# Kernel optimization log

Hardware: AMD Instinct MI355X
Metric: run time of the kernel (lower is better)

The kernel has to match this reference:

```python
import jax, jax.numpy as jnp
import numpy as np

N_NODES = 100000
N_EDGES = 3200000
DIM_IN = 256
DIM_OUT = 256


def setup_inputs() -> dict:
    key = jax.random.key(0)
    k1, k2, k3, k4, k5 = jax.random.split(key, 5)
    x = jax.random.normal(k1, (N_NODES, DIM_IN), dtype=jnp.float32)
    adj_rows = jax.random.randint(k2, (N_EDGES,), 0, N_NODES, dtype=jnp.int64)
    adj_cols = jax.random.randint(k3, (N_EDGES,), 0, N_NODES, dtype=jnp.int64)
    adj_vals = jax.random.uniform(k4, (N_EDGES,), dtype=jnp.float32)
    # torch Linear weight: [dim_out, dim_in]
    W = jax.random.normal(k5, (DIM_OUT, DIM_IN), dtype=jnp.float32) * (1.0 / np.sqrt(DIM_IN))
    return {"x": x, "adj_rows": adj_rows, "adj_cols": adj_cols, "adj_vals": adj_vals, "W": W}


def reference(x, adj_rows, adj_cols, adj_vals, W):
    # h = Linear(x) with no bias -> x @ W.T  : [N, dim_out]
    h = jnp.einsum('nd,od->no', x, W)
    # sparse.mm(adjacency, h): out[r] = sum_{edges e with row r} val[e] * h[col[e]]
    msgs = adj_vals[:, None] * h[adj_cols]            # [E, dim_out]
    out = jax.ops.segment_sum(msgs, adj_rows, num_segments=N_NODES)
    return out
```

## Files before the change

### kernel.cpp

```cpp
#include <hip/hip_runtime.h>
#include <hip/hip_bf16.h>

#define DIM 256
#define GRP 8
#define CAP8 88
#define OVF_CAP 65536

typedef short s16x8 __attribute__((ext_vector_type(8)));
typedef float f32x4 __attribute__((ext_vector_type(4)));

__device__ inline unsigned short f32_bf16_rne(float f) {
    unsigned u = __float_as_uint(f);
    u += 0x7FFFu + ((u >> 16) & 1u);
    return (unsigned short)(u >> 16);
}
__device__ inline float bf16_f32(unsigned short h) {
    return __uint_as_float(((unsigned)h) << 16);
}
__device__ inline float4 bf16x4_f32(uint2 p) {
    float4 r;
    r.x = __uint_as_float(p.x << 16);
    r.y = __uint_as_float(p.x & 0xFFFF0000u);
    r.z = __uint_as_float(p.y << 16);
    r.w = __uint_as_float(p.y & 0xFFFF0000u);
    return r;
}

__global__ __launch_bounds__(256) void prep_w(const float* __restrict__ W,
                                              unsigned short* __restrict__ Wh) {
    int i = blockIdx.x * 256 + threadIdx.x;
    Wh[i] = f32_bf16_rne(W[i]);
}

__global__ __launch_bounds__(256) void gemm_mfma(const float* __restrict__ X,
                                                 const unsigned short* __restrict__ Wh,
                                                 unsigned short* __restrict__ H, int N) {
    __shared__ __align__(16) unsigned short xh[64 * 32];
    __shared__ __align__(16) unsigned short xl[64 * 32];

    const int tid = threadIdx.x;
    const int lane = tid & 63;
    const int wv = tid >> 6;
    const int bm = blockIdx.x * 64;

    const int srow = tid & 63;
    const int schunk = tid >> 6;
    const int grow = bm + srow;
    const bool rowok = grow < N;
    const float* xsrc = X + (size_t)grow * DIM + schunk * 8;
    const int swch = srow * 4 + (schunk ^ ((srow >> 1) & 3));

    const int frow = lane & 15;
    const int fch = lane >> 4;

    f32x4 acc[4][4] = {};

    for (int k0 = 0; k0 < DIM; k0 += 32) {
        float v[8];
        if (rowok) {
            float4 a = *(const float4*)(xsrc + k0);
            float4 b = *(const float4*)(xsrc + k0 + 4);
            v[0] = a.x; v[1] = a.y; v[2] = a.z; v[3] = a.w;
            v[4] = b.x; v[5] = b.y; v[6] = b.z; v[7] = b.w;
        } else {
#pragma unroll
            for (int e = 0; e < 8; ++e) v[e] = 0.f;
        }
        unsigned hh[8], ll[8];
#pragma unroll
        for (int e = 0; e < 8; ++e) {
            unsigned short hu = f32_bf16_rne(v[e]);
            hh[e] = hu;
            ll[e] = f32_bf16_rne(v[e] - bf16_f32(hu));
        }
        uint4 hv = make_uint4(hh[0] | (hh[1] << 16), hh[2] | (hh[3] << 16),
                              hh[4] | (hh[5] << 16), hh[6] | (hh[7] << 16));
        uint4 lv = make_uint4(ll[0] | (ll[1] << 16), ll[2] | (ll[3] << 16),
                              ll[4] | (ll[5] << 16), ll[6] | (ll[7] << 16));
        ((uint4*)xh)[swch] = hv;
        ((uint4*)xl)[swch] = lv;
        __syncthreads();

        s16x8 ah[4], al[4], bh[4];
#pragma unroll
        for (int i = 0; i < 4; ++i) {
            int row = i * 16 + frow;
            int rch = row * 4 + (fch ^ ((row >> 1) & 3));
            ah[i] = __builtin_bit_cast(s16x8, ((const uint4*)xh)[rch]);
            al[i] = __builtin_bit_cast(s16x8, ((const uint4*)xl)[rch]);
        }
#pragma unroll
        for (int j = 0; j < 4; ++j) {
            size_t off = (size_t)(wv * 64 + j * 16 + frow) * DIM + k0 + fch * 8;
            bh[j] = __builtin_bit_cast(s16x8, *(const uint4*)(Wh + off));
        }
#pragma unroll
        for (int i = 0; i < 4; ++i)
#pragma unroll
            for (int j = 0; j < 4; ++j) {
                acc[i][j] = __builtin_amdgcn_mfma_f32_16x16x32_bf16(ah[i], bh[j], acc[i][j], 0, 0, 0);
                acc[i][j] = __builtin_amdgcn_mfma_f32_16x16x32_bf16(al[i], bh[j], acc[i][j], 0, 0, 0);
            }
        __syncthreads();
    }

#pragma unroll
    for (int i = 0; i < 4; ++i)
#pragma unroll
        for (int r = 0; r < 4; ++r) {
            int row = bm + i * 16 + fch * 4 + r;
            if (row < N) {
#pragma unroll
                for (int j = 0; j < 4; ++j)
                    H[(size_t)row * DIM + wv * 64 + j * 16 + frow] = f32_bf16_rne(acc[i][j][r]);
            }
        }
}

__global__ __launch_bounds__(256) void scatter_bucket8(const int* __restrict__ rows,
                                                       const int* __restrict__ cols,
                                                       const float* __restrict__ vals,
                                                       int* __restrict__ cur,
                                                       unsigned long long* __restrict__ buckets,
                                                       uint4* __restrict__ ovf,
                                                       int* __restrict__ ovf_cnt,
                                                       int nE, int B8) {
    unsigned xcd;
    asm volatile("s_getreg_b32 %0, hwreg(HW_REG_XCC_ID)" : "=s"(xcd));
    xcd &= 7;

    int i = blockIdx.x * 256 + threadIdx.x;
    int st = gridDim.x * 256;
    for (int e = i; e < nE; e += st) {
        int r = rows[e];
        unsigned c = (unsigned)cols[e];
        unsigned vb = __float_as_uint(vals[e]);
        int cell = (int)xcd * B8 + (r >> 3);
        int p = atomicAdd(&cur[cell], 1);
        if (p < CAP8) {
            unsigned lo = c | ((unsigned)(r & 7) << 17);
            buckets[(size_t)cell * CAP8 + p] = (unsigned long long)lo | ((unsigned long long)vb << 32);
        } else {
            int q = atomicAdd(ovf_cnt, 1);
            if (q < OVF_CAP) ovf[q] = make_uint4((unsigned)r, c, vb, 0u);
        }
    }
}

__global__ __launch_bounds__(512) void bucket_agg8(const unsigned short* __restrict__ hb,
                                                   const unsigned long long* __restrict__ buckets,
                                                   const int* __restrict__ cur,
                                                   float* __restrict__ out, int N, int B8) {
    const int lane = threadIdx.x & 63;
    const int g = (blockIdx.x * 512 + threadIdx.x) >> 6;
    if (g >= B8) return;

    f32x4 a0 = {0,0,0,0}, a1 = {0,0,0,0}, a2 = {0,0,0,0}, a3 = {0,0,0,0};
    f32x4 a4 = {0,0,0,0}, a5 = {0,0,0,0}, a6 = {0,0,0,0}, a7 = {0,0,0,0};

#define ACCUM(e, gth)                                                        \
    {                                                                        \
        float vv = __uint_as_float((unsigned)((e) >> 32));                   \
        int idx = (int)(((unsigned)(e) >> 17) & 7u);                         \
        float4 f = bf16x4_f32(gth);                                          \
        f32x4 d = {vv * f.x, vv * f.y, vv * f.z, vv * f.w};                  \
        switch (idx) {                                                       \
            case 0: a0 += d; break;  case 1: a1 += d; break;                 \
            case 2: a2 += d; break;  case 3: a3 += d; break;                 \
            case 4: a4 += d; break;  case 5: a5 += d; break;                 \
            case 6: a6 += d; break;  default: a7 += d; break;                \
        }                                                                    \
    }

    for (int x = 0; x < 8; ++x) {
        const int cell = x * B8 + g;
        const int cnt = min(cur[cell], CAP8);
        const unsigned long long* p = buckets + (size_t)cell * CAP8;

        int j = 0;
        for (; j + 4 <= cnt; j += 4) {
            unsigned long long e0 = __builtin_nontemporal_load(p + j);
            unsigned long long e1 = __builtin_nontemporal_load(p + j + 1);
            unsigned long long e2 = __builtin_nontemporal_load(p + j + 2);
            unsigned long long e3 = __builtin_nontemporal_load(p + j + 3);
            uint2 g0 = *(const uint2*)(hb + (size_t)((unsigned)e0 & 0x1FFFFu) * DIM + lane * 4);
            uint2 g1 = *(const uint2*)(hb + (size_t)((unsigned)e1 & 0x1FFFFu) * DIM + lane * 4);
            uint2 g2 = *(const uint2*)(hb + (size_t)((unsigned)e2 & 0x1FFFFu) * DIM + lane * 4);
            uint2 g3 = *(const uint2*)(hb + (size_t)((unsigned)e3 & 0x1FFFFu) * DIM + lane * 4);
            ACCUM(e0, g0) ACCUM(e1, g1) ACCUM(e2, g2) ACCUM(e3, g3)
        }
        for (; j < cnt; ++j) {
            unsigned long long e = __builtin_nontemporal_load(p + j);
            uint2 gv = *(const uint2*)(hb + (size_t)((unsigned)e & 0x1FFFFu) * DIM + lane * 4);
            ACCUM(e, gv)
        }
    }
#undef ACCUM

    const int r0 = g * GRP;
#define STORE_ROW(i, acc) \
    { int r = r0 + (i); if (r < N) __builtin_nontemporal_store(acc, (f32x4*)(out + (size_t)r * DIM + lane * 4)); }
    STORE_ROW(0, a0) STORE_ROW(1, a1) STORE_ROW(2, a2) STORE_ROW(3, a3)
    STORE_ROW(4, a4) STORE_ROW(5, a5) STORE_ROW(6, a6) STORE_ROW(7, a7)
#undef STORE_ROW
}

__global__ __launch_bounds__(256) void ovf_fix(const unsigned short* __restrict__ hb,
                                               const uint4* __restrict__ ovf,
                                               const int* __restrict__ ovf_cnt,
                                               float* __restrict__ out) {
    const int n = min(*ovf_cnt, OVF_CAP);
    const int lane = threadIdx.x & 63;
    const int w = (blockIdx.x * 256 + threadIdx.x) >> 6;
    const int nw = gridDim.x * 4;
    for (int e = w; e < n; e += nw) {
        uint4 t = ovf[e];
        float vv = __uint_as_float(t.z);
        float4 f = bf16x4_f32(*(const uint2*)(hb + (size_t)t.y * DIM + lane * 4));
        float* op = out + (size_t)t.x * DIM + lane * 4;
        atomicAdd(op + 0, vv * f.x);
        atomicAdd(op + 1, vv * f.y);
        atomicAdd(op + 2, vv * f.z);
        atomicAdd(op + 3, vv * f.w);
    }
}

__global__ __launch_bounds__(256) void edge_scatter(const unsigned short* __restrict__ hb,
                                                    const int* __restrict__ rows,
                                                    const int* __restrict__ cols,
                                                    const float* __restrict__ vals,
                                                    float* __restrict__ out, int nE) {
    const int lane = threadIdx.x & 63;
    const int wave = (blockIdx.x * blockDim.x + threadIdx.x) >> 6;
    const int nWaves = (gridDim.x * blockDim.x) >> 6;
    for (int e = wave; e < nE; e += nWaves) {
        const int r = rows[e];
        const int c = cols[e];
        const float v = vals[e];
        float4 f = bf16x4_f32(*(const uint2*)(hb + (size_t)c * DIM + lane * 4));
        float* op = out + (size_t)r * DIM + lane * 4;
        atomicAdd(op + 0, v * f.x);
        atomicAdd(op + 1, v * f.y);
        atomicAdd(op + 2, v * f.z);
        atomicAdd(op + 3, v * f.w);
    }
}

extern "C" void kernel_launch(void* const* d_in, const int* in_sizes, int n_in,
                              void* d_out, int out_size, void* d_ws, size_t ws_size,
                              hipStream_t stream) {
    const float* x    = (const float*)d_in[0];
    const int*   rows = (const int*)d_in[1];
    const int*   cols = (const int*)d_in[2];
    const float* vals = (const float*)d_in[3];
    const float* W    = (const float*)d_in[4];

    float* out = (float*)d_out;
    const int N  = in_sizes[0] / DIM;
    const int nE = in_sizes[1];
    const int B8 = (N + GRP - 1) / GRP;
    const int cells = 8 * B8;

    auto align256 = [](size_t v) { return (v + 255) & ~(size_t)255; };
    char* ws = (char*)d_ws;

    size_t off_wh   = 0;
    size_t off_h    = align256(off_wh + (size_t)DIM * DIM * 2);
    size_t off_cur  = align256(off_h + (size_t)N * DIM * 2);
    size_t off_ovf  = align256(off_cur + (size_t)(cells + 64) * 4);
    size_t off_bkt  = align256(off_ovf + (size_t)OVF_CAP * 16);
    size_t total    = off_bkt + (size_t)cells * CAP8 * 8;

    unsigned short* Wh = (unsigned short*)(ws + off_wh);
    unsigned short* h  = (unsigned short*)(ws + off_h);

    const bool packOK = (N <= (1 << 17));

    prep_w<<<DIM * DIM / 256, 256, 0, stream>>>(W, Wh);

    if (ws_size >= total && packOK) {
        int*   cur     = (int*)(ws + off_cur);
        int*   ovf_cnt = cur + cells;
        uint4* ovf     = (uint4*)(ws + off_ovf);
        unsigned long long* bkt = (unsigned long long*)(ws + off_bkt);

        hipMemsetAsync(cur, 0, (size_t)(cells + 64) * 4, stream);
        scatter_bucket8<<<2048, 256, 0, stream>>>(rows, cols, vals, cur, bkt, ovf, ovf_cnt, nE, B8);

        gemm_mfma<<<(N + 63) / 64, 256, 0, stream>>>(x, Wh, h, N);

        bucket_agg8<<<(B8 + 7) / 8, 512, 0, stream>>>(h, bkt, cur, out, N, B8);
        ovf_fix<<<32, 256, 0, stream>>>(h, ovf, ovf_cnt, out);
    } else {
        gemm_mfma<<<(N + 63) / 64, 256, 0, stream>>>(x, Wh, h, N);
        hipMemsetAsync(out, 0, (size_t)out_size * sizeof(float), stream);
        edge_scatter<<<2048, 256, 0, stream>>>(h, rows, cols, vals, out, nE);
    }
}
```

Measured before the change: 506.9 us.

## Split each row-group's aggregation across two wavefronts with LDS reduction

The bucket aggregation kernel now assigns two wavefronts per 8-row group, each processing half of the eight XCD bucket cells. The partial accumulators are combined through a 32KB shared-memory buffer before the final store. The gather loop is also unrolled from 4 to 8 edges so more loads are in flight. This doubles wave-level parallelism for the latency-bound gather, at the cost of LDS use that may limit occupancy, an extra block barrier, and more register pressure from the deeper unroll.

Result: no change. 512.7 us (+1.1%).

```diff
diff --git a/kernel.cpp b/kernel.cpp
--- a/kernel.cpp
+++ b/kernel.cpp
@@ -147,13 +147,18 @@
     }
 }
 
-__global__ __launch_bounds__(512) void bucket_agg8(const unsigned short* __restrict__ hb,
-                                                   const unsigned long long* __restrict__ buckets,
-                                                   const int* __restrict__ cur,
-                                                   float* __restrict__ out, int N, int B8) {
-    const int lane = threadIdx.x & 63;
-    const int g = (blockIdx.x * 512 + threadIdx.x) >> 6;
-    if (g >= B8) return;
+__global__ __launch_bounds__(512) void bucket_agg8s(const unsigned short* __restrict__ hb,
+                                                    const unsigned long long* __restrict__ buckets,
+                                                    const int* __restrict__ cur,
+                                                    float* __restrict__ out, int N, int B8) {
+    __shared__ float red[4][GRP][DIM];
+    const int tid = threadIdx.x;
+    const int lane = tid & 63;
+    const int wid = tid >> 6;
+    const int gl = wid >> 1;
+    const int half = wid & 1;
+    const int g = blockIdx.x * 4 + gl;
+    const bool active = g < B8;
 
     f32x4 a0 = {0,0,0,0}, a1 = {0,0,0,0}, a2 = {0,0,0,0}, a3 = {0,0,0,0};
     f32x4 a4 = {0,0,0,0}, a5 = {0,0,0,0}, a6 = {0,0,0,0}, a7 = {0,0,0,0};
@@ -172,37 +177,65 @@
         }                                                                    \
     }
 
-    for (int x = 0; x < 8; ++x) {
-        const int cell = x * B8 + g;
-        const int cnt = min(cur[cell], CAP8);
-        const unsigned long long* p = buckets + (size_t)cell * CAP8;
-
-        int j = 0;
-        for (; j + 4 <= cnt; j += 4) {
-            unsigned long long e0 = __builtin_nontemporal_load(p + j);
-            unsigned long long e1 = __builtin_nontemporal_load(p + j + 1);
-            unsigned long long e2 = __builtin_nontemporal_load(p + j + 2);
-            unsigned long long e3 = __builtin_nontemporal_load(p + j + 3);
-            uint2 g0 = *(const uint2*)(hb + (size_t)((unsigned)e0 & 0x1FFFFu) * DIM + lane * 4);
-            uint2 g1 = *(const uint2*)(hb + (size_t)((unsigned)e1 & 0x1FFFFu) * DIM + lane * 4);
-            uint2 g2 = *(const uint2*)(hb + (size_t)((unsigned)e2 & 0x1FFFFu) * DIM + lane * 4);
-            uint2 g3 = *(const uint2*)(hb + (size_t)((unsigned)e3 & 0x1FFFFu) * DIM + lane * 4);
-            ACCUM(e0, g0) ACCUM(e1, g1) ACCUM(e2, g2) ACCUM(e3, g3)
-        }
-        for (; j < cnt; ++j) {
-            unsigned long long e = __builtin_nontemporal_load(p + j);
-            uint2 gv = *(const uint2*)(hb + (size_t)((unsigned)e & 0x1FFFFu) * DIM + lane * 4);
-            ACCUM(e, gv)
+    if (active) {
+        for (int xx = 0; xx < 4; ++xx) {
+            const int cell = (half * 4 + xx) * B8 + g;
+            const int cnt = min(cur[cell], CAP8);
+            const unsigned long long* p = buckets + (size_t)cell * CAP8;
+
+            int j = 0;
+            for (; j + 8 <= cnt; j += 8) {
+                unsigned long long e0 = __builtin_nontemporal_load(p + j);
+                unsigned long long e1 = __builtin_nontemporal_load(p + j + 1);
+                unsigned long long e2 = __builtin_nontemporal_load(p + j + 2);
+                unsigned long long e3 = __builtin_nontemporal_load(p + j + 3);
+                unsigned long long e4 = __builtin_nontemporal_load(p + j + 4);
+                unsigned long long e5 = __builtin_nontemporal_load(p + j + 5);
+                unsigned long long e6 = __builtin_nontemporal_load(p + j + 6);
+                unsigned long long e7 = __builtin_nontemporal_load(p + j + 7);
+                uint2 g0 = *(const uint2*)(hb + (size_t)((unsigned)e0 & 0x1FFFFu) * DIM + lane * 4);
+                uint2 g1 = *(const uint2*)(hb + (size_t)((unsigned)e1 & 0x1FFFFu) * DIM + lane * 4);
+                uint2 g2 = *(const uint2*)(hb + (size_t)((unsigned)e2 & 0x1FFFFu) * DIM + lane * 4);
+                uint2 g3 = *(const uint2*)(hb + (size_t)((unsigned)e3 & 0x1FFFFu) * DIM + lane * 4);
+                uint2 g4 = *(const uint2*)(hb + (size_t)((unsigned)e4 & 0x1FFFFu) * DIM + lane * 4);
+                uint2 g5 = *(const uint2*)(hb + (size_t)((unsigned)e5 & 0x1FFFFu) * DIM + lane * 4);
+                uint2 g6 = *(const uint2*)(hb + (size_t)((unsigned)e6 & 0x1FFFFu) * DIM + lane * 4);
+                uint2 g7 = *(const uint2*)(hb + (size_t)((unsigned)e7 & 0x1FFFFu) * DIM + lane * 4);
+                ACCUM(e0, g0) ACCUM(e1, g1) ACCUM(e2, g2) ACCUM(e3, g3)
+                ACCUM(e4, g4) ACCUM(e5, g5) ACCUM(e6, g6) ACCUM(e7, g7)
+            }
+            for (; j < cnt; ++j) {
+                unsigned long long e = __builtin_nontemporal_load(p + j);
+                uint2 gv = *(const uint2*)(hb + (size_t)((unsigned)e & 0x1FFFFu) * DIM + lane * 4);
+                ACCUM(e, gv)
+            }
         }
     }
 #undef ACCUM
 
-    const int r0 = g * GRP;
-#define STORE_ROW(i, acc) \
-    { int r = r0 + (i); if (r < N) __builtin_nontemporal_store(acc, (f32x4*)(out + (size_t)r * DIM + lane * 4)); }
-    STORE_ROW(0, a0) STORE_ROW(1, a1) STORE_ROW(2, a2) STORE_ROW(3, a3)
-    STORE_ROW(4, a4) STORE_ROW(5, a5) STORE_ROW(6, a6) STORE_ROW(7, a7)
-#undef STORE_ROW
+    if (active && half) {
+        float* rb = &red[gl][0][lane * 4];
+#define DUMP(i, acc) *(f32x4*)(rb + (i) * DIM) = acc;
+        DUMP(0, a0) DUMP(1, a1) DUMP(2, a2) DUMP(3, a3)
+        DUMP(4, a4) DUMP(5, a5) DUMP(6, a6) DUMP(7, a7)
+#undef DUMP
+    }
+    __syncthreads();
+    if (active && !half) {
+        const float* rb = &red[gl][0][lane * 4];
+        const int r0 = g * GRP;
+#define FIN(i, acc)                                                              \
+        {                                                                        \
+            int r = r0 + (i);                                                    \
+            if (r < N) {                                                         \
+                f32x4 s = acc + *(const f32x4*)(rb + (i) * DIM);                 \
+                __builtin_nontemporal_store(s, (f32x4*)(out + (size_t)r * DIM + lane * 4)); \
+            }                                                                    \
+        }
+        FIN(0, a0) FIN(1, a1) FIN(2, a2) FIN(3, a3)
+        FIN(4, a4) FIN(5, a5) FIN(6, a6) FIN(7, a7)
+#undef FIN
+    }
 }
 
 __global__ __launch_bounds__(256) void ovf_fix(const unsigned short* __restrict__ hb,
@@ -289,7 +322,7 @@
 
         gemm_mfma<<<(N + 63) / 64, 256, 0, stream>>>(x, Wh, h, N);
 
-        bucket_agg8<<<(B8 + 7) / 8, 512, 0, stream>>>(h, bkt, cur, out, N, B8);
+        bucket_agg8s<<<(B8 + 3) / 4, 512, 0, stream>>>(h, bkt, cur, out, N, B8);
         ovf_fix<<<32, 256, 0, stream>>>(h, ovf, ovf_cnt, out);
     } else {
         gemm_mfma<<<(N + 63) / 64, 256, 0, stream>>>(x, Wh, h, N);
```
